# Optimization experiments

Hardware: AMD Instinct MI355X
Metric: run time of the kernel (lower is better)

## Reference

```python
import jax, jax.numpy as jnp
import numpy as np

N = 8388608  # number of histogram bins (2^23)


def setup_inputs() -> dict:
    key = jax.random.key(0)
    # two histograms on the 1D line; emd2 requires equal total mass -> normalize rows
    x = jax.random.uniform(key, (2, N), dtype=jnp.float32)
    x = x / jnp.sum(x, axis=1, keepdims=True)
    return {"x": x}


def reference(x):
    # Exact optimal transport (EMD) between x[0] and x[1] with ground cost
    # M[i,j] = |i - j| (ot.utils.dist on arange(n) with minkowski metric in 1D).
    # For the 1D line metric the exact EMD has the closed form
    #   EMD = sum_i |CDF_a(i) - CDF_b(i)| * (bin spacing = 1)
    # identical to what the network-simplex solver in ot.emd2 returns.
    cdf_diff = jnp.cumsum(x[0] - x[1])  # [n]; last entry ~0 for equal-mass inputs
    return jnp.sum(jnp.abs(cdf_diff))
```

## Files before the change

### kernel.cpp

```cpp
#include <hip/hip_runtime.h>

#define BLOCK 256
#define CHUNK 4096
#define NITER (CHUNK / (BLOCK * 4))
#define NBLK 2048

__device__ __forceinline__ float wave_incl_scan(float v, int lane) {
#pragma unroll
    for (int off = 1; off < 64; off <<= 1) {
        float u = __shfl_up(v, off);
        if (lane >= off) v += u;
    }
    return v;
}

__device__ __forceinline__ float wave_reduce(float v) {
#pragma unroll
    for (int off = 32; off >= 1; off >>= 1) v += __shfl_down(v, off);
    return v;
}

__global__ __launch_bounds__(BLOCK) void k_partial(const float* __restrict__ x0,
                                                   const float* __restrict__ x1,
                                                   float* __restrict__ partials,
                                                   int n) {
    const int t = threadIdx.x;
    const int lane = t & 63;
    const int wave = t >> 6;
    const long base = (long)blockIdx.x * CHUNK;
    float s = 0.f;
#pragma unroll
    for (int k = 0; k < NITER; ++k) {
        long idx = base + (long)(k * BLOCK + t) * 4;
        if (idx + 3 < n) {
            float4 a = *reinterpret_cast<const float4*>(x0 + idx);
            float4 b = *reinterpret_cast<const float4*>(x1 + idx);
            s += (a.x - b.x) + (a.y - b.y) + (a.z - b.z) + (a.w - b.w);
        } else {
#pragma unroll
            for (int j = 0; j < 4; ++j) {
                long i = idx + j;
                if (i < n) s += x0[i] - x1[i];
            }
        }
    }
    s = wave_reduce(s);
    __shared__ float ws[BLOCK / 64];
    if (lane == 0) ws[wave] = s;
    __syncthreads();
    if (t == 0) {
        float tot = 0.f;
#pragma unroll
        for (int w = 0; w < BLOCK / 64; ++w) tot += ws[w];
        partials[blockIdx.x] = tot;
        if (blockIdx.x == 0) *(float*)(partials + NBLK) = 0.f;
    }
}

__global__ __launch_bounds__(BLOCK) void k_emd(const float* __restrict__ x0,
                                               const float* __restrict__ x1,
                                               const float* __restrict__ partials,
                                               float* __restrict__ out, int n) {
    const int t = threadIdx.x;
    const int lane = t & 63;
    const int wave = t >> 6;
    const int bid = blockIdx.x;
    const long base = (long)bid * CHUNK;

    __shared__ float red[BLOCK / 64];
    __shared__ float wsum[BLOCK / 64];


    float s = 0.f;
    for (int j = 0; j < NBLK / BLOCK; ++j) {
        int i = j * BLOCK + t;
        if (i < bid) s += partials[i];
    }
    s = wave_reduce(s);
    if (lane == 0) red[wave] = s;
    __syncthreads();
    float excl = 0.f;
#pragma unroll
    for (int w = 0; w < BLOCK / 64; ++w) excl += red[w];

    float acc = 0.f;
    float run = excl;
#pragma unroll
    for (int k = 0; k < NITER; ++k) {
        long idx = base + (long)(k * BLOCK + t) * 4;
        float d0 = 0.f, d1 = 0.f, d2 = 0.f, d3 = 0.f;
        if (idx + 3 < n) {
            float4 a = *reinterpret_cast<const float4*>(x0 + idx);
            float4 b = *reinterpret_cast<const float4*>(x1 + idx);
            d0 = a.x - b.x; d1 = a.y - b.y; d2 = a.z - b.z; d3 = a.w - b.w;
        } else {
            if (idx + 0 < n) d0 = x0[idx + 0] - x1[idx + 0];
            if (idx + 1 < n) d1 = x0[idx + 1] - x1[idx + 1];
            if (idx + 2 < n) d2 = x0[idx + 2] - x1[idx + 2];
            if (idx + 3 < n) d3 = x0[idx + 3] - x1[idx + 3];
        }
        float p0 = d0, p1 = p0 + d1, p2 = p1 + d2, p3 = p2 + d3;
        float inc = wave_incl_scan(p3, lane);
        if (lane == 63) wsum[wave] = inc;
        __syncthreads();
        float wexcl = 0.f, ctot = 0.f;
#pragma unroll
        for (int w = 0; w < BLOCK / 64; ++w) {
            float v = wsum[w];
            ctot += v;
            if (w < wave) wexcl += v;
        }
        float boff = run + wexcl + (inc - p3);
        if (idx + 0 < n) acc += fabsf(boff + p0);
        if (idx + 1 < n) acc += fabsf(boff + p1);
        if (idx + 2 < n) acc += fabsf(boff + p2);
        if (idx + 3 < n) acc += fabsf(boff + p3);
        run += ctot;
        __syncthreads();
    }
    acc = wave_reduce(acc);
    if (lane == 0) red[wave] = acc;
    __syncthreads();
    if (t == 0) {
        float tot = 0.f;
#pragma unroll
        for (int w = 0; w < BLOCK / 64; ++w) tot += red[w];
        atomicAdd(out, tot);
    }
}

extern "C" void kernel_launch(void* const* d_in, const int* in_sizes, int n_in,
                              void* d_out, int out_size, void* d_ws, size_t ws_size,
                              hipStream_t stream) {
    const float* x = (const float*)d_in[0];
    const int total = in_sizes[0];
    const int n = total / 2;
    const float* x0 = x;
    const float* x1 = x + n;
    float* out = (float*)d_out;
    float* partials = (float*)d_ws;

    hipMemsetAsync(out, 0, sizeof(float), stream);
    k_partial<<<NBLK, BLOCK, 0, stream>>>(x0, x1, partials, n);
    k_emd<<<NBLK, BLOCK, 0, stream>>>(x0, x1, partials, out, n);
}
```

Measured before the change: 122.1 us.

## Preload scan inputs and batch wave scans behind one barrier; fold memset into kernel

The EMD pass now issues all of a thread's float4 loads up front, before reading the prefix partials. It then runs every per-iteration wave scan and records the segment totals in a shared array indexed by iteration. That replaces two barriers per iteration with a single barrier, so load latency can overlap and blocks stall less. The separate memset of the output is removed; block 0 of the first kernel zeroes it instead, and the grid size is derived from n. The cost is more registers and shared memory held per thread, which could lower occupancy.

```diff
diff --git a/kernel.cpp b/kernel.cpp
--- a/kernel.cpp
+++ b/kernel.cpp
@@ -23,11 +23,12 @@
 __global__ __launch_bounds__(BLOCK) void k_partial(const float* __restrict__ x0,
                                                    const float* __restrict__ x1,
                                                    float* __restrict__ partials,
-                                                   int n) {
+                                                   float* __restrict__ out, int n) {
     const int t = threadIdx.x;
     const int lane = t & 63;
     const int wave = t >> 6;
     const long base = (long)blockIdx.x * CHUNK;
+    if (blockIdx.x == 0 && t == 0) *out = 0.f;
     float s = 0.f;
 #pragma unroll
     for (int k = 0; k < NITER; ++k) {
@@ -53,7 +54,6 @@
 #pragma unroll
         for (int w = 0; w < BLOCK / 64; ++w) tot += ws[w];
         partials[blockIdx.x] = tot;
-        if (blockIdx.x == 0) *(float*)(partials + NBLK) = 0.f;
     }
 }
 
@@ -68,17 +68,49 @@
     const long base = (long)bid * CHUNK;
 
     __shared__ float red[BLOCK / 64];
-    __shared__ float wsum[BLOCK / 64];
+    __shared__ float seg[NITER][BLOCK / 64];
+    __shared__ float wacc[BLOCK / 64];
 
+    float4 va[NITER], vb[NITER];
+#pragma unroll
+    for (int k = 0; k < NITER; ++k) {
+        long idx = base + (long)(k * BLOCK + t) * 4;
+        if (idx + 3 < n) {
+            va[k] = *reinterpret_cast<const float4*>(x0 + idx);
+            vb[k] = *reinterpret_cast<const float4*>(x1 + idx);
+        } else {
+            float4 a = {0.f, 0.f, 0.f, 0.f}, b = {0.f, 0.f, 0.f, 0.f};
+            if (idx + 0 < n) { a.x = x0[idx + 0]; b.x = x1[idx + 0]; }
+            if (idx + 1 < n) { a.y = x0[idx + 1]; b.y = x1[idx + 1]; }
+            if (idx + 2 < n) { a.z = x0[idx + 2]; b.z = x1[idx + 2]; }
+            va[k] = a; vb[k] = b;
+        }
+    }
 
     float s = 0.f;
-    for (int j = 0; j < NBLK / BLOCK; ++j) {
+    for (int j = 0; j * BLOCK < (int)gridDim.x; ++j) {
         int i = j * BLOCK + t;
         if (i < bid) s += partials[i];
     }
     s = wave_reduce(s);
     if (lane == 0) red[wave] = s;
+
+    float p[NITER][4], tincl[NITER];
+#pragma unroll
+    for (int k = 0; k < NITER; ++k) {
+        float d0 = va[k].x - vb[k].x;
+        float d1 = va[k].y - vb[k].y;
+        float d2 = va[k].z - vb[k].z;
+        float d3 = va[k].w - vb[k].w;
+        p[k][0] = d0;
+        p[k][1] = p[k][0] + d1;
+        p[k][2] = p[k][1] + d2;
+        p[k][3] = p[k][2] + d3;
+        tincl[k] = wave_incl_scan(p[k][3], lane);
+        if (lane == 63) seg[k][wave] = tincl[k];
+    }
     __syncthreads();
+
     float excl = 0.f;
 #pragma unroll
     for (int w = 0; w < BLOCK / 64; ++w) excl += red[w];
@@ -87,44 +119,29 @@
     float run = excl;
 #pragma unroll
     for (int k = 0; k < NITER; ++k) {
-        long idx = base + (long)(k * BLOCK + t) * 4;
-        float d0 = 0.f, d1 = 0.f, d2 = 0.f, d3 = 0.f;
-        if (idx + 3 < n) {
-            float4 a = *reinterpret_cast<const float4*>(x0 + idx);
-            float4 b = *reinterpret_cast<const float4*>(x1 + idx);
-            d0 = a.x - b.x; d1 = a.y - b.y; d2 = a.z - b.z; d3 = a.w - b.w;
-        } else {
-            if (idx + 0 < n) d0 = x0[idx + 0] - x1[idx + 0];
-            if (idx + 1 < n) d1 = x0[idx + 1] - x1[idx + 1];
-            if (idx + 2 < n) d2 = x0[idx + 2] - x1[idx + 2];
-            if (idx + 3 < n) d3 = x0[idx + 3] - x1[idx + 3];
-        }
-        float p0 = d0, p1 = p0 + d1, p2 = p1 + d2, p3 = p2 + d3;
-        float inc = wave_incl_scan(p3, lane);
-        if (lane == 63) wsum[wave] = inc;
-        __syncthreads();
-        float wexcl = 0.f, ctot = 0.f;
+        float woff = 0.f, ktot = 0.f;
 #pragma unroll
         for (int w = 0; w < BLOCK / 64; ++w) {
-            float v = wsum[w];
-            ctot += v;
-            if (w < wave) wexcl += v;
+            float v = seg[k][w];
+            ktot += v;
+            if (w < wave) woff += v;
         }
-        float boff = run + wexcl + (inc - p3);
-        if (idx + 0 < n) acc += fabsf(boff + p0);
-        if (idx + 1 < n) acc += fabsf(boff + p1);
-        if (idx + 2 < n) acc += fabsf(boff + p2);
-        if (idx + 3 < n) acc += fabsf(boff + p3);
-        run += ctot;
-        __syncthreads();
+        float boff = run + woff + (tincl[k] - p[k][3]);
+        long idx = base + (long)(k * BLOCK + t) * 4;
+        if (idx + 0 < n) acc += fabsf(boff + p[k][0]);
+        if (idx + 1 < n) acc += fabsf(boff + p[k][1]);
+        if (idx + 2 < n) acc += fabsf(boff + p[k][2]);
+        if (idx + 3 < n) acc += fabsf(boff + p[k][3]);
+        run += ktot;
     }
+
     acc = wave_reduce(acc);
-    if (lane == 0) red[wave] = acc;
+    if (lane == 0) wacc[wave] = acc;
     __syncthreads();
     if (t == 0) {
         float tot = 0.f;
 #pragma unroll
-        for (int w = 0; w < BLOCK / 64; ++w) tot += red[w];
+        for (int w = 0; w < BLOCK / 64; ++w) tot += wacc[w];
         atomicAdd(out, tot);
     }
 }
@@ -140,7 +157,8 @@
     float* out = (float*)d_out;
     float* partials = (float*)d_ws;
 
-    hipMemsetAsync(out, 0, sizeof(float), stream);
-    k_partial<<<NBLK, BLOCK, 0, stream>>>(x0, x1, partials, n);
-    k_emd<<<NBLK, BLOCK, 0, stream>>>(x0, x1, partials, out, n);
+    const int B = (n + CHUNK - 1) / CHUNK;
+
+    k_partial<<<B, BLOCK, 0, stream>>>(x0, x1, partials, out, n);
+    k_emd<<<B, BLOCK, 0, stream>>>(x0, x1, partials, out, n);
 }
```

Result: no change. 121.8 us (-0.2%).

## Fuse partial-sum and scan kernels into one pass with grid-wide barrier

Applied to the files above, without the earlier changes.

Merges the two passes into a single kernel. Each block loads its chunk once and keeps the per-thread prefix values in registers, publishes its block total, then waits on a global atomic counter until every block has arrived before computing its exclusive offset. This removes the second read of both input arrays and one kernel launch. In exchange it relies on all blocks being co-resident (1024 blocks, 8 per CU via launch bounds), since otherwise the spin barrier would deadlock. Chunk size also doubles, which raises register pressure per thread.

```diff
diff --git a/kernel.cpp b/kernel.cpp
--- a/kernel.cpp
+++ b/kernel.cpp
@@ -1,9 +1,9 @@
 #include <hip/hip_runtime.h>
 
 #define BLOCK 256
-#define CHUNK 4096
+#define CHUNK 8192
 #define NITER (CHUNK / (BLOCK * 4))
-#define NBLK 2048
+#define MAXB 4096
 
 __device__ __forceinline__ float wave_incl_scan(float v, int lane) {
 #pragma unroll
@@ -20,71 +20,26 @@
     return v;
 }
 
-__global__ __launch_bounds__(BLOCK) void k_partial(const float* __restrict__ x0,
-                                                   const float* __restrict__ x1,
-                                                   float* __restrict__ partials,
-                                                   int n) {
-    const int t = threadIdx.x;
-    const int lane = t & 63;
-    const int wave = t >> 6;
-    const long base = (long)blockIdx.x * CHUNK;
-    float s = 0.f;
-#pragma unroll
-    for (int k = 0; k < NITER; ++k) {
-        long idx = base + (long)(k * BLOCK + t) * 4;
-        if (idx + 3 < n) {
-            float4 a = *reinterpret_cast<const float4*>(x0 + idx);
-            float4 b = *reinterpret_cast<const float4*>(x1 + idx);
-            s += (a.x - b.x) + (a.y - b.y) + (a.z - b.z) + (a.w - b.w);
-        } else {
-#pragma unroll
-            for (int j = 0; j < 4; ++j) {
-                long i = idx + j;
-                if (i < n) s += x0[i] - x1[i];
-            }
-        }
-    }
-    s = wave_reduce(s);
-    __shared__ float ws[BLOCK / 64];
-    if (lane == 0) ws[wave] = s;
-    __syncthreads();
-    if (t == 0) {
-        float tot = 0.f;
-#pragma unroll
-        for (int w = 0; w < BLOCK / 64; ++w) tot += ws[w];
-        partials[blockIdx.x] = tot;
-        if (blockIdx.x == 0) *(float*)(partials + NBLK) = 0.f;
-    }
-}
-
-__global__ __launch_bounds__(BLOCK) void k_emd(const float* __restrict__ x0,
-                                               const float* __restrict__ x1,
-                                               const float* __restrict__ partials,
-                                               float* __restrict__ out, int n) {
+__global__ __launch_bounds__(BLOCK, 8) void k_emd_fused(
+    const float* __restrict__ x0, const float* __restrict__ x1,
+    unsigned* __restrict__ counter, float* __restrict__ partials,
+    float* __restrict__ out, int n) {
     const int t = threadIdx.x;
     const int lane = t & 63;
     const int wave = t >> 6;
     const int bid = blockIdx.x;
+    const int B = gridDim.x;
     const long base = (long)bid * CHUNK;
 
+    __shared__ float seg[NITER][BLOCK / 64];
     __shared__ float red[BLOCK / 64];
-    __shared__ float wsum[BLOCK / 64];
 
+    if (bid == 0 && t == 0)
+        __hip_atomic_store(out, 0.f, __ATOMIC_RELAXED, __HIP_MEMORY_SCOPE_AGENT);
 
-    float s = 0.f;
-    for (int j = 0; j < NBLK / BLOCK; ++j) {
-        int i = j * BLOCK + t;
-        if (i < bid) s += partials[i];
-    }
-    s = wave_reduce(s);
-    if (lane == 0) red[wave] = s;
-    __syncthreads();
-    float excl = 0.f;
-#pragma unroll
-    for (int w = 0; w < BLOCK / 64; ++w) excl += red[w];
+    float p[NITER][4];
+    float texcl[NITER];
 
-    float acc = 0.f;
-    float run = excl;
 #pragma unroll
     for (int k = 0; k < NITER; ++k) {
         long idx = base + (long)(k * BLOCK + t) * 4;
@@ -99,26 +54,70 @@
             if (idx + 2 < n) d2 = x0[idx + 2] - x1[idx + 2];
             if (idx + 3 < n) d3 = x0[idx + 3] - x1[idx + 3];
         }
-        float p0 = d0, p1 = p0 + d1, p2 = p1 + d2, p3 = p2 + d3;
-        float inc = wave_incl_scan(p3, lane);
-        if (lane == 63) wsum[wave] = inc;
-        __syncthreads();
-        float wexcl = 0.f, ctot = 0.f;
+        p[k][0] = d0;
+        p[k][1] = p[k][0] + d1;
+        p[k][2] = p[k][1] + d2;
+        p[k][3] = p[k][2] + d3;
+        float inc = wave_incl_scan(p[k][3], lane);
+        texcl[k] = inc - p[k][3];
+        if (lane == 63) seg[k][wave] = inc;
+    }
+    __syncthreads();
+
+    float aggregate = 0.f;
+#pragma unroll
+    for (int k = 0; k < NITER; ++k)
+#pragma unroll
+        for (int w = 0; w < BLOCK / 64; ++w) aggregate += seg[k][w];
+
+    if (t == 0) {
+        __hip_atomic_store(&partials[bid], aggregate, __ATOMIC_RELAXED,
+                           __HIP_MEMORY_SCOPE_AGENT);
+        __hip_atomic_fetch_add(counter, 1u, __ATOMIC_RELEASE,
+                               __HIP_MEMORY_SCOPE_AGENT);
+        while (__hip_atomic_load(counter, __ATOMIC_ACQUIRE,
+                                 __HIP_MEMORY_SCOPE_AGENT) < (unsigned)B)
+            __builtin_amdgcn_s_sleep(2);
+    }
+    __syncthreads();
+
+    float s = 0.f;
+#pragma unroll
+    for (int j = 0; j < MAXB / BLOCK; ++j) {
+        int i = j * BLOCK + t;
+        if (i < bid)
+            s += __hip_atomic_load(&partials[i], __ATOMIC_RELAXED,
+                                   __HIP_MEMORY_SCOPE_AGENT);
+    }
+    s = wave_reduce(s);
+    if (lane == 0) red[wave] = s;
+    __syncthreads();
+    float excl = 0.f;
+#pragma unroll
+    for (int w = 0; w < BLOCK / 64; ++w) excl += red[w];
+
+    float acc = 0.f;
+    float run = excl;
+#pragma unroll
+    for (int k = 0; k < NITER; ++k) {
+        float woff = 0.f, ktot = 0.f;
 #pragma unroll
         for (int w = 0; w < BLOCK / 64; ++w) {
-            float v = wsum[w];
-            ctot += v;
-            if (w < wave) wexcl += v;
+            float v = seg[k][w];
+            ktot += v;
+            if (w < wave) woff += v;
         }
-        float boff = run + wexcl + (inc - p3);
-        if (idx + 0 < n) acc += fabsf(boff + p0);
-        if (idx + 1 < n) acc += fabsf(boff + p1);
-        if (idx + 2 < n) acc += fabsf(boff + p2);
-        if (idx + 3 < n) acc += fabsf(boff + p3);
-        run += ctot;
-        __syncthreads();
+        float boff = run + woff + texcl[k];
+        long idx = base + (long)(k * BLOCK + t) * 4;
+        if (idx + 0 < n) acc += fabsf(boff + p[k][0]);
+        if (idx + 1 < n) acc += fabsf(boff + p[k][1]);
+        if (idx + 2 < n) acc += fabsf(boff + p[k][2]);
+        if (idx + 3 < n) acc += fabsf(boff + p[k][3]);
+        run += ktot;
     }
+
     acc = wave_reduce(acc);
+    __syncthreads();
     if (lane == 0) red[wave] = acc;
     __syncthreads();
     if (t == 0) {
@@ -138,9 +137,12 @@
     const float* x0 = x;
     const float* x1 = x + n;
     float* out = (float*)d_out;
-    float* partials = (float*)d_ws;
 
-    hipMemsetAsync(out, 0, sizeof(float), stream);
-    k_partial<<<NBLK, BLOCK, 0, stream>>>(x0, x1, partials, n);
-    k_emd<<<NBLK, BLOCK, 0, stream>>>(x0, x1, partials, out, n);
+    unsigned* counter = (unsigned*)d_ws;
+    float* partials = (float*)((char*)d_ws + 256);
+
+    const int B = (n + CHUNK - 1) / CHUNK;
+
+    hipMemsetAsync(d_ws, 0, 256, stream);
+    k_emd_fused<<<B, BLOCK, 0, stream>>>(x0, x1, counter, partials, out, n);
 }
```

New measurement: 251.2 us. +105.7%, slower.
